# Kernel tuning notes

Hardware: AMD Instinct MI355X
Metric: run time of the kernel (lower is better)

Reference implementation:

```python
import jax, jax.numpy as jnp
import numpy as np

B, H, W = 64, 512, 512
NC = 19  # Cityscapes classes


def setup_inputs() -> dict:
    key = jax.random.key(0)
    k1, k2 = jax.random.split(key)
    pred = jax.random.randint(k1, (B, H, W), 0, NC, dtype=jnp.int32)
    # gt class labels include the don't-care index NC; stored as float segmaps in [0,1]
    gt_cls = jax.random.randint(k2, (B, 1, H, W), 0, NC + 1, dtype=jnp.int32)
    segmaps = gt_cls.astype(jnp.float32) / 255.0
    return {"pred": pred, "segmaps": segmaps, "n_classes": NC, "use_dont_care": 1}


def reference(pred, segmaps, n_classes, use_dont_care):
    # gt = (segmaps * 255).long(); nearest-interp to (H,W) is identity here (same res)
    gt = (segmaps * 255.0).astype(jnp.int32)[:, 0]  # [B,H,W]
    ignore_idx = n_classes if use_dont_care else -1
    keep = gt != ignore_idx  # [B,H,W] bool
    nc2 = n_classes * n_classes
    b = pred.shape[0]
    # merged pair index; masked-out pixels contribute weight 0 at bin 0
    merge = jnp.where(keep, pred * n_classes + gt, 0)  # [B,H,W]
    offsets = (jnp.arange(b, dtype=jnp.int32) * nc2)[:, None, None]
    idx = (merge + offsets).reshape(-1)  # flatten: one fused histogram over whole batch
    w = keep.astype(jnp.int32).reshape(-1)
    hist = jnp.zeros((b * nc2,), dtype=jnp.int32).at[idx].add(w)
    return hist.reshape(b, n_classes, n_classes)
```

## Files before the change

### kernel.cpp

```cpp
#include <hip/hip_runtime.h>


#define NC2C  361
#define SLOT  362
#define WPB   8
#define BPB   32

__global__ __launch_bounds__(256) void zero_out_kernel(int* __restrict__ out, int n) {
    int i = blockIdx.x * 256 + threadIdx.x;
    if (i < n) out[i] = 0;
}

__device__ __forceinline__ unsigned pix_bin(int pe, float se, int nc, int nc2,
                                            int ignore) {
    int g = (int)(se * 255.0f);
    unsigned b = (unsigned)(pe * nc + g);
    b = (g == ignore) ? (unsigned)nc2 : b;
    b = b < (unsigned)nc2 ? b : (unsigned)nc2;
    return b;
}

__device__ __forceinline__ int byte_sum8(const unsigned* __restrict__ w) {
    int s = 0;
    #pragma unroll
    for (int j = 0; j < WPB; ++j) {
        unsigned u = w[j];
        s += (int)(u & 0xffu) + (int)((u >> 8) & 0xffu)
           + (int)((u >> 16) & 0xffu) + (int)(u >> 24);
    }
    return s;
}

__global__ __launch_bounds__(256) void seg_hist_part(
    const int* __restrict__ pred,
    const float* __restrict__ seg,
    const int* __restrict__ ncls_p,
    const int* __restrict__ udc_p,
    int* __restrict__ partials,
    int npix_per_batch)
{
    __shared__ unsigned hist[SLOT * WPB];

    const int nc = ncls_p[0];
    const int nc2 = nc * nc;
    const int ignore = udc_p[0] ? nc : -1;

    const int b = blockIdx.y;
    const int tid = threadIdx.x;
    const int lane = tid & 63;

    for (int i = tid; i < SLOT * WPB; i += 256) hist[i] = 0;
    __syncthreads();

    const unsigned wslot = (unsigned)(lane & 7);
    const unsigned inc = 1u << (8 * ((lane >> 3) & 3));

    const size_t base = (size_t)b * (size_t)npix_per_batch;
    const int4*   p4 = (const int4*)(pred + base);
    const float4* s4 = (const float4*)(seg + base);
    const int nvec = npix_per_batch >> 2;
    const int stride = BPB * 256;

    for (int i = blockIdx.x * 256 + tid; i < nvec; i += stride) {
        int4   p = p4[i];
        float4 s = s4[i];
        unsigned b0 = pix_bin(p.x, s.x, nc, nc2, ignore);
        unsigned b1 = pix_bin(p.y, s.y, nc, nc2, ignore);
        unsigned b2 = pix_bin(p.z, s.z, nc, nc2, ignore);
        unsigned b3 = pix_bin(p.w, s.w, nc, nc2, ignore);
        atomicAdd(&hist[b0 * WPB + wslot], inc);
        atomicAdd(&hist[b1 * WPB + wslot], inc);
        atomicAdd(&hist[b2 * WPB + wslot], inc);
        atomicAdd(&hist[b3 * WPB + wslot], inc);
    }
    __syncthreads();

    int* pout = partials + ((size_t)b * BPB + blockIdx.x) * (size_t)nc2;
    for (int k = tid; k < nc2; k += 256) {
        pout[k] = byte_sum8(&hist[k * WPB]);
    }
}

__global__ __launch_bounds__(256) void reduce_part(
    const int* __restrict__ partials, int* __restrict__ out, int nc2)
{
    const int b = blockIdx.x;
    const int* p = partials + (size_t)b * BPB * (size_t)nc2;
    for (int bin = threadIdx.x; bin < nc2; bin += 256) {
        int sum = 0;
        #pragma unroll 8
        for (int j = 0; j < BPB; ++j) sum += p[(size_t)j * nc2 + bin];
        out[(size_t)b * nc2 + bin] = sum;
    }
}

__global__ __launch_bounds__(256) void seg_hist_atomic(
    const int* __restrict__ pred, const float* __restrict__ seg,
    const int* __restrict__ ncls_p, const int* __restrict__ udc_p,
    int* __restrict__ out, int npix_per_batch)
{
    __shared__ unsigned hist[SLOT * WPB];
    const int nc = ncls_p[0];
    const int nc2 = nc * nc;
    const int ignore = udc_p[0] ? nc : -1;
    const int b = blockIdx.y;
    const int tid = threadIdx.x;
    const int lane = tid & 63;
    for (int i = tid; i < SLOT * WPB; i += 256) hist[i] = 0;
    __syncthreads();
    const unsigned wslot = (unsigned)(lane & 7);
    const unsigned inc = 1u << (8 * ((lane >> 3) & 3));
    const size_t base = (size_t)b * (size_t)npix_per_batch;
    const int4*   p4 = (const int4*)(pred + base);
    const float4* s4 = (const float4*)(seg + base);
    const int nvec = npix_per_batch >> 2;
    for (int i = blockIdx.x * 256 + tid; i < nvec; i += BPB * 256) {
        int4 p = p4[i];
        float4 s = s4[i];
        unsigned b0 = pix_bin(p.x, s.x, nc, nc2, ignore);
        unsigned b1 = pix_bin(p.y, s.y, nc, nc2, ignore);
        unsigned b2 = pix_bin(p.z, s.z, nc, nc2, ignore);
        unsigned b3 = pix_bin(p.w, s.w, nc, nc2, ignore);
        atomicAdd(&hist[b0 * WPB + wslot], inc);
        atomicAdd(&hist[b1 * WPB + wslot], inc);
        atomicAdd(&hist[b2 * WPB + wslot], inc);
        atomicAdd(&hist[b3 * WPB + wslot], inc);
    }
    __syncthreads();
    int* gout = out + (size_t)b * (size_t)nc2;
    for (int k = tid; k < nc2; k += 256) {
        int v = byte_sum8(&hist[k * WPB]);
        if (v) atomicAdd(&gout[k], v);
    }
}

extern "C" void kernel_launch(void* const* d_in, const int* in_sizes, int n_in,
                              void* d_out, int out_size, void* d_ws, size_t ws_size,
                              hipStream_t stream) {
    const int*   pred = (const int*)d_in[0];
    const float* seg  = (const float*)d_in[1];
    const int*   ncp  = (const int*)d_in[2];
    const int*   udp  = (const int*)d_in[3];
    int* out = (int*)d_out;

    const int total_pix = in_sizes[0];
    const int B = out_size / NC2C;
    const int npix_per_batch = total_pix / B;
    const int nc2 = out_size / B;

    const size_t ws_needed = (size_t)B * BPB * nc2 * sizeof(int);

    if (ws_size >= ws_needed) {
        int* partials = (int*)d_ws;
        dim3 grid(BPB, B);
        seg_hist_part<<<grid, 256, 0, stream>>>(pred, seg, ncp, udp, partials,
                                                npix_per_batch);
        reduce_part<<<B, 256, 0, stream>>>(partials, out, nc2);
    } else {
        int nblk = (out_size + 255) / 256;
        zero_out_kernel<<<nblk, 256, 0, stream>>>(out, out_size);
        dim3 grid(BPB, B);
        seg_hist_atomic<<<grid, 256, 0, stream>>>(pred, seg, ncp, udp, out,
                                                  npix_per_batch);
    }
}
```

Measured before the change: 153.4 us.

## Replace shared atomics with per-thread private byte histograms in LDS

Each thread now owns a private 8-bit histogram row in shared memory and bumps it with plain loads and stores instead of shared atomics. Block size drops to 128 threads and blocks per batch to 12, and loads are software-pipelined two iterations ahead. A column-sum pass reads two bins at a time to build the per-block partials. This removes atomic contention, but per-thread byte counters can overflow if a thread handles more than 255 pixels. The large LDS footprint per block also limits occupancy.

After: 156.4 us. Within noise of the previous version (+2.0%).

```diff
diff --git a/kernel.cpp b/kernel.cpp
--- a/kernel.cpp
+++ b/kernel.cpp
@@ -1,10 +1,11 @@
 #include <hip/hip_runtime.h>
 
 
-#define NC2C  361
-#define SLOT  362
-#define WPB   8
-#define BPB   32
+#define NC2C    361
+#define SLOTB   362
+#define RSTRIDE 364
+#define TPB     128
+#define BPBn    12
 
 __global__ __launch_bounds__(256) void zero_out_kernel(int* __restrict__ out, int n) {
     int i = blockIdx.x * 256 + threadIdx.x;
@@ -20,18 +21,19 @@
     return b;
 }
 
-__device__ __forceinline__ int byte_sum8(const unsigned* __restrict__ w) {
-    int s = 0;
-    #pragma unroll
-    for (int j = 0; j < WPB; ++j) {
-        unsigned u = w[j];
-        s += (int)(u & 0xffu) + (int)((u >> 8) & 0xffu)
-           + (int)((u >> 16) & 0xffu) + (int)(u >> 24);
-    }
-    return s;
+__device__ __forceinline__ void bump4(unsigned char* __restrict__ mine,
+                                      int4 p, float4 s, int nc, int nc2, int ignore) {
+    unsigned b0 = pix_bin(p.x, s.x, nc, nc2, ignore);
+    unsigned b1 = pix_bin(p.y, s.y, nc, nc2, ignore);
+    unsigned b2 = pix_bin(p.z, s.z, nc, nc2, ignore);
+    unsigned b3 = pix_bin(p.w, s.w, nc, nc2, ignore);
+    mine[b0] = (unsigned char)(mine[b0] + 1);
+    mine[b1] = (unsigned char)(mine[b1] + 1);
+    mine[b2] = (unsigned char)(mine[b2] + 1);
+    mine[b3] = (unsigned char)(mine[b3] + 1);
 }
 
-__global__ __launch_bounds__(256) void seg_hist_part(
+__global__ __launch_bounds__(TPB) void seg_hist_part(
     const int* __restrict__ pred,
     const float* __restrict__ seg,
     const int* __restrict__ ncls_p,
@@ -39,7 +41,8 @@
     int* __restrict__ partials,
     int npix_per_batch)
 {
-    __shared__ unsigned hist[SLOT * WPB];
+    __shared__ unsigned int hist32[(TPB * RSTRIDE) / 4];
+    unsigned char* h8 = (unsigned char*)hist32;
 
     const int nc = ncls_p[0];
     const int nc2 = nc * nc;
@@ -47,37 +50,52 @@
 
     const int b = blockIdx.y;
     const int tid = threadIdx.x;
-    const int lane = tid & 63;
 
-    for (int i = tid; i < SLOT * WPB; i += 256) hist[i] = 0;
+    for (int i = tid; i < (TPB * RSTRIDE) / 4; i += TPB) hist32[i] = 0;
     __syncthreads();
 
-    const unsigned wslot = (unsigned)(lane & 7);
-    const unsigned inc = 1u << (8 * ((lane >> 3) & 3));
+    unsigned char* mine = h8 + tid * RSTRIDE;
 
     const size_t base = (size_t)b * (size_t)npix_per_batch;
     const int4*   p4 = (const int4*)(pred + base);
     const float4* s4 = (const float4*)(seg + base);
     const int nvec = npix_per_batch >> 2;
-    const int stride = BPB * 256;
+    const int stride = BPBn * TPB;
 
-    for (int i = blockIdx.x * 256 + tid; i < nvec; i += stride) {
-        int4   p = p4[i];
-        float4 s = s4[i];
-        unsigned b0 = pix_bin(p.x, s.x, nc, nc2, ignore);
-        unsigned b1 = pix_bin(p.y, s.y, nc, nc2, ignore);
-        unsigned b2 = pix_bin(p.z, s.z, nc, nc2, ignore);
-        unsigned b3 = pix_bin(p.w, s.w, nc, nc2, ignore);
-        atomicAdd(&hist[b0 * WPB + wslot], inc);
-        atomicAdd(&hist[b1 * WPB + wslot], inc);
-        atomicAdd(&hist[b2 * WPB + wslot], inc);
-        atomicAdd(&hist[b3 * WPB + wslot], inc);
+    const int i0 = blockIdx.x * TPB + tid;
+    const int niter = (i0 < nvec) ? (nvec - 1 - i0) / stride + 1 : 0;
+
+    if (niter >= 2) {
+        int4   pa = p4[i0];          float4 sa = s4[i0];
+        int4   pb = p4[i0 + stride]; float4 sb = s4[i0 + stride];
+        int inext = i0 + 2 * stride;
+        for (int t = 0; t < niter - 2; ++t, inext += stride) {
+            int4   pc_ = p4[inext];
+            float4 sc_ = s4[inext];
+            bump4(mine, pa, sa, nc, nc2, ignore);
+            pa = pb; sa = sb;
+            pb = pc_; sb = sc_;
+        }
+        bump4(mine, pa, sa, nc, nc2, ignore);
+        bump4(mine, pb, sb, nc, nc2, ignore);
+    } else if (niter == 1) {
+        bump4(mine, p4[i0], s4[i0], nc, nc2, ignore);
     }
     __syncthreads();
 
-    int* pout = partials + ((size_t)b * BPB + blockIdx.x) * (size_t)nc2;
-    for (int k = tid; k < nc2; k += 256) {
-        pout[k] = byte_sum8(&hist[k * WPB]);
+    int* pout = partials + ((size_t)b * BPBn + blockIdx.x) * (size_t)nc2;
+    const int npair = (nc2 + 2) / 2;
+    for (int pr = tid; pr < npair; pr += TPB) {
+        int k0 = 2 * pr;
+        int sum0 = 0, sum1 = 0;
+        #pragma unroll 8
+        for (int t = 0; t < TPB; ++t) {
+            unsigned v = *(const unsigned short*)(h8 + t * RSTRIDE + k0);
+            sum0 += (int)(v & 0xffu);
+            sum1 += (int)(v >> 8);
+        }
+        pout[k0] = sum0;
+        if (k0 + 1 < nc2) pout[k0 + 1] = sum1;
     }
 }
 
@@ -85,52 +103,50 @@
     const int* __restrict__ partials, int* __restrict__ out, int nc2)
 {
     const int b = blockIdx.x;
-    const int* p = partials + (size_t)b * BPB * (size_t)nc2;
+    const int* p = partials + (size_t)b * BPBn * (size_t)nc2;
     for (int bin = threadIdx.x; bin < nc2; bin += 256) {
         int sum = 0;
-        #pragma unroll 8
-        for (int j = 0; j < BPB; ++j) sum += p[(size_t)j * nc2 + bin];
+        #pragma unroll
+        for (int j = 0; j < BPBn; ++j) sum += p[(size_t)j * nc2 + bin];
         out[(size_t)b * nc2 + bin] = sum;
     }
 }
 
-__global__ __launch_bounds__(256) void seg_hist_atomic(
+__global__ __launch_bounds__(TPB) void seg_hist_atomic(
     const int* __restrict__ pred, const float* __restrict__ seg,
     const int* __restrict__ ncls_p, const int* __restrict__ udc_p,
     int* __restrict__ out, int npix_per_batch)
 {
-    __shared__ unsigned hist[SLOT * WPB];
+    __shared__ unsigned int hist32[(TPB * RSTRIDE) / 4];
+    unsigned char* h8 = (unsigned char*)hist32;
     const int nc = ncls_p[0];
     const int nc2 = nc * nc;
     const int ignore = udc_p[0] ? nc : -1;
     const int b = blockIdx.y;
     const int tid = threadIdx.x;
-    const int lane = tid & 63;
-    for (int i = tid; i < SLOT * WPB; i += 256) hist[i] = 0;
+    for (int i = tid; i < (TPB * RSTRIDE) / 4; i += TPB) hist32[i] = 0;
     __syncthreads();
-    const unsigned wslot = (unsigned)(lane & 7);
-    const unsigned inc = 1u << (8 * ((lane >> 3) & 3));
+    unsigned char* mine = h8 + tid * RSTRIDE;
     const size_t base = (size_t)b * (size_t)npix_per_batch;
     const int4*   p4 = (const int4*)(pred + base);
     const float4* s4 = (const float4*)(seg + base);
     const int nvec = npix_per_batch >> 2;
-    for (int i = blockIdx.x * 256 + tid; i < nvec; i += BPB * 256) {
-        int4 p = p4[i];
-        float4 s = s4[i];
-        unsigned b0 = pix_bin(p.x, s.x, nc, nc2, ignore);
-        unsigned b1 = pix_bin(p.y, s.y, nc, nc2, ignore);
-        unsigned b2 = pix_bin(p.z, s.z, nc, nc2, ignore);
-        unsigned b3 = pix_bin(p.w, s.w, nc, nc2, ignore);
-        atomicAdd(&hist[b0 * WPB + wslot], inc);
-        atomicAdd(&hist[b1 * WPB + wslot], inc);
-        atomicAdd(&hist[b2 * WPB + wslot], inc);
-        atomicAdd(&hist[b3 * WPB + wslot], inc);
+    for (int i = blockIdx.x * TPB + tid; i < nvec; i += BPBn * TPB) {
+        bump4(mine, p4[i], s4[i], nc, nc2, ignore);
     }
     __syncthreads();
     int* gout = out + (size_t)b * (size_t)nc2;
-    for (int k = tid; k < nc2; k += 256) {
-        int v = byte_sum8(&hist[k * WPB]);
-        if (v) atomicAdd(&gout[k], v);
+    const int npair = (nc2 + 2) / 2;
+    for (int pr = tid; pr < npair; pr += TPB) {
+        int k0 = 2 * pr;
+        int sum0 = 0, sum1 = 0;
+        for (int t = 0; t < TPB; ++t) {
+            unsigned v = *(const unsigned short*)(h8 + t * RSTRIDE + k0);
+            sum0 += (int)(v & 0xffu);
+            sum1 += (int)(v >> 8);
+        }
+        if (sum0) atomicAdd(&gout[k0], sum0);
+        if (k0 + 1 < nc2 && sum1) atomicAdd(&gout[k0 + 1], sum1);
     }
 }
 
@@ -148,19 +164,19 @@
     const int npix_per_batch = total_pix / B;
     const int nc2 = out_size / B;
 
-    const size_t ws_needed = (size_t)B * BPB * nc2 * sizeof(int);
+    const size_t ws_needed = (size_t)B * BPBn * nc2 * sizeof(int);
 
     if (ws_size >= ws_needed) {
         int* partials = (int*)d_ws;
-        dim3 grid(BPB, B);
-        seg_hist_part<<<grid, 256, 0, stream>>>(pred, seg, ncp, udp, partials,
+        dim3 grid(BPBn, B);
+        seg_hist_part<<<grid, TPB, 0, stream>>>(pred, seg, ncp, udp, partials,
                                                 npix_per_batch);
         reduce_part<<<B, 256, 0, stream>>>(partials, out, nc2);
     } else {
         int nblk = (out_size + 255) / 256;
         zero_out_kernel<<<nblk, 256, 0, stream>>>(out, out_size);
-        dim3 grid(BPB, B);
-        seg_hist_atomic<<<grid, 256, 0, stream>>>(pred, seg, ncp, udp, out,
+        dim3 grid(BPBn, B);
+        seg_hist_atomic<<<grid, TPB, 0, stream>>>(pred, seg, ncp, udp, out,
                                                   npix_per_batch);
     }
 }
```
